# Optimization experiments

Hardware: AMD Instinct MI355X
Metric: run time of the kernel (lower is better)

## Reference

```python
import jax, jax.numpy as jnp
import numpy as np

EPS_KERNEL = 1e-6
EPS_Z = 1e-6


def softmax_kernel(data, projection_matrix):
    # data: [b,h,l,d], projection_matrix: [m,d]
    data_normalizer = data.shape[-1] ** (-0.25)
    data = data * data_normalizer
    projection = jnp.einsum('bhld,md->bhlm', data, projection_matrix)
    data_squared_norm = jnp.sum(data ** 2, axis=-1, keepdims=True) / 2
    return jnp.exp(projection - data_squared_norm + EPS_KERNEL)


def setup_inputs() -> dict:
    key = jax.random.key(0)
    k1, k2, k3, k4 = jax.random.split(key, 4)
    b, h, l, d, m = 4, 8, 8192, 64, 256
    return {
        'q': jax.random.normal(k1, (b, h, l, d), dtype=jnp.float32),
        'k': jax.random.normal(k2, (b, h, l, d), dtype=jnp.float32),
        'v': jax.random.normal(k3, (b, h, l, d), dtype=jnp.float32),
        'projection_matrix': jax.random.normal(k4, (m, d), dtype=jnp.float32),
    }


def reference(q, k, v, projection_matrix):
    q_prime = softmax_kernel(q, projection_matrix)  # [b,h,l,m]
    k_prime = softmax_kernel(k, projection_matrix)  # [b,h,l,m]
    kv = jnp.einsum('bhlm,bhld->bhmd', k_prime, v)  # [b,h,m,d]
    k_sum = jnp.sum(k_prime, axis=2)                # [b,h,m]
    z_raw = jnp.einsum('bhlm,bhm->bhl', q_prime, k_sum)
    z = 1.0 / (z_raw + EPS_Z)                       # [b,h,l]
    # (q_prime @ kv) scaled per-token by z
    out = jnp.einsum('bhlm,bhmd->bhld', q_prime, kv) * z[..., None]
    return out
```

## Files before the change

### kernel.cpp

```cpp
#include <hip/hip_runtime.h>
#include <hip/hip_bf16.h>


#define BH 32
#define LL 8192
#define DD 64
#define MM 256
#define NRM 0.35355339059327373f
#define SQS 0.0625f
#define EPSK 1e-6f
#define EPSZ 1e-6f
#define NTILE 8
#define RPB 256

typedef __attribute__((ext_vector_type(8))) short bf16x8;
typedef __attribute__((ext_vector_type(4))) float f32x4;
#define MFMA(a, b, c) __builtin_amdgcn_mfma_f32_16x16x32_bf16(a, b, c, 0, 0, 0)

static __device__ __forceinline__ short f2bf(float x) {
    union { float f; unsigned u; } c{x};
    unsigned r = c.u + 0x7fffu + ((c.u >> 16) & 1u);
    return (short)(r >> 16);
}

static __device__ __forceinline__ void decode_block(int i, int& bh, int& chunk) {
    bh = ((i & 7) << 2) | ((i >> 3) & 3);
    chunk = i >> 5;
}

static __device__ __forceinline__ void load_pfrags(
    const float* __restrict__ Pm, int wv, int quad, int l16, bf16x8 pb[2][4])
{
#pragma unroll
    for (int ks = 0; ks < 2; ++ks)
#pragma unroll
        for (int mt = 0; mt < 4; ++mt) {
            const float* pr = Pm + (wv * 64 + mt * 16 + l16) * DD + ks * 32 + quad * 8;
            float4 p0 = *(const float4*)pr;
            float4 p1 = *(const float4*)(pr + 4);
            bf16x8 f;
            f[0] = f2bf(p0.x * NRM); f[1] = f2bf(p0.y * NRM);
            f[2] = f2bf(p0.z * NRM); f[3] = f2bf(p0.w * NRM);
            f[4] = f2bf(p1.x * NRM); f[5] = f2bf(p1.y * NRM);
            f[6] = f2bf(p1.z * NRM); f[7] = f2bf(p1.w * NRM);
            pb[ks][mt] = f;
        }
}

__global__ __launch_bounds__(256, 2) void kv_kernel(
    const float* __restrict__ kin, const float* __restrict__ vin,
    const float* __restrict__ Pm, float* __restrict__ kv, float* __restrict__ ksum)
{
    __shared__ short Kb[32 * 72];
    __shared__ short Vt[64 * 40];
    __shared__ short Ktp[256 * 40];
    __shared__ float cl_lds[32];

    const int t = threadIdx.x;
    const int lane = t & 63, wv = t >> 6;
    const int quad = lane >> 4, l16 = lane & 15;
    const int bh = blockIdx.x >> 4, chunk = blockIdx.x & 15;

    bf16x8 pb[2][4];
    load_pfrags(Pm, wv, quad, l16, pb);

    f32x4 kvacc[4][4];
#pragma unroll
    for (int mt = 0; mt < 4; ++mt)
#pragma unroll
        for (int dt = 0; dt < 4; ++dt) kvacc[mt][dt] = (f32x4)0.f;
    float ksacc[4] = {0.f, 0.f, 0.f, 0.f};

    const size_t base = ((size_t)bh * LL + (size_t)chunk * 512) * DD;
    const float* kb = kin + base;
    const float* vb = vin + base;
    const int sl = t >> 4, sd4 = t & 15;

    for (int tile = 0; tile < 16; ++tile) {
        __syncthreads();
#pragma unroll
        for (int half = 0; half < 2; ++half) {
            const int l = sl + half * 16;
            const int gi = (tile * 32 + l) * DD + sd4 * 4;
            float4 kf = *(const float4*)(kb + gi);
            float sq = kf.x * kf.x + kf.y * kf.y + kf.z * kf.z + kf.w * kf.w;
            sq += __shfl_xor(sq, 1); sq += __shfl_xor(sq, 2);
            sq += __shfl_xor(sq, 4); sq += __shfl_xor(sq, 8);
            if (sd4 == 0) cl_lds[l] = EPSK - SQS * sq;
            union { short s[4]; unsigned long long u; } uk;
            uk.s[0] = f2bf(kf.x); uk.s[1] = f2bf(kf.y);
            uk.s[2] = f2bf(kf.z); uk.s[3] = f2bf(kf.w);
            *(unsigned long long*)&Kb[l * 72 + sd4 * 4] = uk.u;
            float4 vf = *(const float4*)(vb + gi);
            Vt[(sd4 * 4 + 0) * 40 + l] = f2bf(vf.x);
            Vt[(sd4 * 4 + 1) * 40 + l] = f2bf(vf.y);
            Vt[(sd4 * 4 + 2) * 40 + l] = f2bf(vf.z);
            Vt[(sd4 * 4 + 3) * 40 + l] = f2bf(vf.w);
        }
        __syncthreads();
        f32x4 pt[2][4];
#pragma unroll
        for (int lt = 0; lt < 2; ++lt)
#pragma unroll
            for (int mt = 0; mt < 4; ++mt) pt[lt][mt] = (f32x4)0.f;
#pragma unroll
        for (int ks = 0; ks < 2; ++ks)
#pragma unroll
            for (int lt = 0; lt < 2; ++lt) {
                bf16x8 af = *(bf16x8*)&Kb[(lt * 16 + l16) * 72 + ks * 32 + quad * 8];
#pragma unroll
                for (int mt = 0; mt < 4; ++mt)
                    pt[lt][mt] = MFMA(af, pb[ks][mt], pt[lt][mt]);
            }
        float cl[2][4];
#pragma unroll
        for (int lt = 0; lt < 2; ++lt)
#pragma unroll
            for (int r = 0; r < 4; ++r) cl[lt][r] = cl_lds[lt * 16 + quad * 4 + r];
#pragma unroll
        for (int lt = 0; lt < 2; ++lt)
#pragma unroll
            for (int mt = 0; mt < 4; ++mt) {
                union { short s[4]; unsigned long long u; } uo;
#pragma unroll
                for (int r = 0; r < 4; ++r) {
                    float w = __expf(pt[lt][mt][r] + cl[lt][r]);
                    ksacc[mt] += w;
                    uo.s[r] = f2bf(w);
                }
                *(unsigned long long*)&Ktp[(wv * 64 + mt * 16 + l16) * 40 + lt * 16 + quad * 4] = uo.u;
            }
        bf16x8 aK[4], bV[4];
#pragma unroll
        for (int mt = 0; mt < 4; ++mt)
            aK[mt] = *(bf16x8*)&Ktp[(wv * 64 + mt * 16 + l16) * 40 + quad * 8];
#pragma unroll
        for (int dt = 0; dt < 4; ++dt)
            bV[dt] = *(bf16x8*)&Vt[(dt * 16 + l16) * 40 + quad * 8];
#pragma unroll
        for (int mt = 0; mt < 4; ++mt)
#pragma unroll
            for (int dt = 0; dt < 4; ++dt)
                kvacc[mt][dt] = MFMA(aK[mt], bV[dt], kvacc[mt][dt]);
    }
    float* kvg = kv + (size_t)bh * MM * DD;
#pragma unroll
    for (int mt = 0; mt < 4; ++mt) {
        float r = ksacc[mt];
        r += __shfl_xor(r, 16); r += __shfl_xor(r, 32);
        if (quad == 0) atomicAdd(ksum + bh * MM + wv * 64 + mt * 16 + l16, r);
#pragma unroll
        for (int dt = 0; dt < 4; ++dt)
#pragma unroll
            for (int rg = 0; rg < 4; ++rg)
                atomicAdd(kvg + (wv * 64 + mt * 16 + quad * 4 + rg) * DD + dt * 16 + l16,
                          kvacc[mt][dt][rg]);
    }
}

__global__ __launch_bounds__(256, 4) void out_kernel(
    const float* __restrict__ qin, const float* __restrict__ Pm,
    const float* __restrict__ kv, const float* __restrict__ ksum,
    float* __restrict__ out)
{
    __shared__ short sm[64 * 264];
    __shared__ short Qb[32 * 72];
    __shared__ float ks_lds[MM];
    __shared__ float cl_lds[32];
    __shared__ float z_lds[32];

    const int t = threadIdx.x;
    const int lane = t & 63, wv = t >> 6;
    const int quad = lane >> 4, l16 = lane & 15;
    int bh, chunk;
    decode_block(blockIdx.x, bh, chunk);

    bf16x8 pb[2][4];
    load_pfrags(Pm, wv, quad, l16, pb);

    const float* kvg = kv + (size_t)bh * MM * DD;
#pragma unroll
    for (int it = 0; it < 16; ++it) {
        const int i = t + it * 256;
        const int m = i >> 4, d4 = i & 15;
        const float4 f = *(const float4*)(kvg + m * DD + d4 * 4);
        sm[(d4 * 4 + 0) * 264 + m] = f2bf(f.x);
        sm[(d4 * 4 + 1) * 264 + m] = f2bf(f.y);
        sm[(d4 * 4 + 2) * 264 + m] = f2bf(f.z);
        sm[(d4 * 4 + 3) * 264 + m] = f2bf(f.w);
    }
    ks_lds[t] = ksum[bh * MM + t];
    __syncthreads();

    bf16x8 bk[8];
#pragma unroll
    for (int ks = 0; ks < 8; ++ks)
        bk[ks] = *(const bf16x8*)&sm[(wv * 16 + l16) * 264 + ks * 32 + quad * 8];

    const size_t base = ((size_t)bh * LL + (size_t)chunk * RPB) * DD;
    const float* qb = qin + base;
    float* ob = out + base;
    const int sl = t >> 4, sd4 = t & 15;

    float4 qreg[2];
#pragma unroll
    for (int half = 0; half < 2; ++half)
        qreg[half] = *(const float4*)(qb + (sl + half * 16) * DD + sd4 * 4);

    for (int tile = 0; tile < NTILE; ++tile) {
        __syncthreads();
        if (t < 32) z_lds[t] = 0.f;
#pragma unroll
        for (int half = 0; half < 2; ++half) {
            const int l = sl + half * 16;
            const float4 qf = qreg[half];
            float sq = qf.x * qf.x + qf.y * qf.y + qf.z * qf.z + qf.w * qf.w;
            sq += __shfl_xor(sq, 1); sq += __shfl_xor(sq, 2);
            sq += __shfl_xor(sq, 4); sq += __shfl_xor(sq, 8);
            if (sd4 == 0) cl_lds[l] = EPSK - SQS * sq;
            union { short s[4]; unsigned long long u; } uq;
            uq.s[0] = f2bf(qf.x); uq.s[1] = f2bf(qf.y);
            uq.s[2] = f2bf(qf.z); uq.s[3] = f2bf(qf.w);
            *(unsigned long long*)&Qb[l * 72 + sd4 * 4] = uq.u;
        }
        if (tile + 1 < NTILE) {
#pragma unroll
            for (int half = 0; half < 2; ++half)
                qreg[half] = *(const float4*)(qb + ((tile + 1) * 32 + sl + half * 16) * DD + sd4 * 4);
        }
        __syncthreads();

        bf16x8 qf2[2][2];
#pragma unroll
        for (int ks2 = 0; ks2 < 2; ++ks2)
#pragma unroll
            for (int lt = 0; lt < 2; ++lt)
                qf2[ks2][lt] = *(const bf16x8*)&Qb[(lt * 16 + l16) * 72 + ks2 * 32 + quad * 8];
        const float clv0 = cl_lds[l16];
        const float clv1 = cl_lds[16 + l16];
        float zp0 = 0.f, zp1 = 0.f;
#pragma unroll
        for (int mt = 0; mt < 4; ++mt) {
            f32x4 pt0 = (f32x4)0.f, pt1 = (f32x4)0.f;
#pragma unroll
            for (int ks2 = 0; ks2 < 2; ++ks2) {
                pt0 = MFMA(pb[ks2][mt], qf2[ks2][0], pt0);
                pt1 = MFMA(pb[ks2][mt], qf2[ks2][1], pt1);
            }
            const float4 km4 = *(const float4*)&ks_lds[wv * 64 + mt * 16 + quad * 4];
            const float km[4] = {km4.x, km4.y, km4.z, km4.w};
            union { short s[4]; unsigned long long u; } u0, u1;
#pragma unroll
            for (int r = 0; r < 4; ++r) {
                const float w0 = __expf(pt0[r] + clv0);
                const float w1 = __expf(pt1[r] + clv1);
                zp0 += w0 * km[r];
                zp1 += w1 * km[r];
                u0.s[r] = f2bf(w0);
                u1.s[r] = f2bf(w1);
            }
            *(unsigned long long*)&sm[(l16) * 264 + wv * 64 + mt * 16 + quad * 4] = u0.u;
            *(unsigned long long*)&sm[(16 + l16) * 264 + wv * 64 + mt * 16 + quad * 4] = u1.u;
        }
        zp0 += __shfl_xor(zp0, 16); zp0 += __shfl_xor(zp0, 32);
        zp1 += __shfl_xor(zp1, 16); zp1 += __shfl_xor(zp1, 32);
        if (lane < 16) {
            atomicAdd(&z_lds[l16], zp0);
            atomicAdd(&z_lds[16 + l16], zp1);
        }
        __syncthreads();

        f32x4 oc0 = (f32x4)0.f, oc1 = (f32x4)0.f;
#pragma unroll
        for (int ks = 0; ks < 8; ++ks) {
            const bf16x8 aq0 = *(const bf16x8*)&sm[(l16) * 264 + ks * 32 + quad * 8];
            const bf16x8 aq1 = *(const bf16x8*)&sm[(16 + l16) * 264 + ks * 32 + quad * 8];
            oc0 = MFMA(aq0, bk[ks], oc0);
            oc1 = MFMA(aq1, bk[ks], oc1);
        }
#pragma unroll
        for (int r = 0; r < 4; ++r) {
            const int row0 = quad * 4 + r;
            const float z0 = 1.f / (z_lds[row0] + EPSZ);
            ob[(size_t)(tile * 32 + row0) * DD + wv * 16 + l16] = oc0[r] * z0;
            const int row1 = 16 + quad * 4 + r;
            const float z1 = 1.f / (z_lds[row1] + EPSZ);
            ob[(size_t)(tile * 32 + row1) * DD + wv * 16 + l16] = oc1[r] * z1;
        }
    }
}

extern "C" void kernel_launch(void* const* d_in, const int* in_sizes, int n_in,
                              void* d_out, int out_size, void* d_ws, size_t ws_size,
                              hipStream_t stream) {
    const float* q  = (const float*)d_in[0];
    const float* k  = (const float*)d_in[1];
    const float* v  = (const float*)d_in[2];
    const float* Pm = (const float*)d_in[3];

    float* kvw = (float*)d_ws;
    float* ksw = kvw + (size_t)BH * MM * DD;

    hipMemsetAsync(d_ws, 0, ((size_t)BH * MM * DD + (size_t)BH * MM) * sizeof(float), stream);
    hipLaunchKernelGGL(kv_kernel, dim3(512), dim3(256), 0, stream, k, v, Pm, kvw, ksw);
    hipLaunchKernelGGL(out_kernel, dim3(1024), dim3(256), 0, stream, q, Pm, kvw, ksw, (float*)d_out);
}
```

Baseline: 327.0 us.

## Replace atomic kv accumulation with per-block partials and a reduction kernel

Each kv block now writes its partial kv and k_sum results to a dedicated workspace slice instead of accumulating into a zeroed buffer. A separate reduce kernel then sums the 16 chunk partials per head. This removes the memset and the contended global accumulation. The cost is an extra kernel launch and significant extra global memory traffic for the partials. The new path only runs when the workspace is large enough, otherwise it falls back to the old path.

```diff
diff --git a/kernel.cpp b/kernel.cpp
--- a/kernel.cpp
+++ b/kernel.cpp
@@ -13,6 +13,13 @@
 #define NTILE 8
 #define RPB 256
 
+#define NBLK_A 512
+#define KVP_SZ ((size_t)NBLK_A * MM * DD)
+#define KSP_SZ ((size_t)NBLK_A * MM)
+#define KVF_SZ ((size_t)BH * MM * DD)
+#define KSF_SZ ((size_t)BH * MM)
+#define WS_NEED_BYTES ((KVP_SZ + KSP_SZ + KVF_SZ + KSF_SZ) * sizeof(float))
+
 typedef __attribute__((ext_vector_type(8))) short bf16x8;
 typedef __attribute__((ext_vector_type(4))) float f32x4;
 #define MFMA(a, b, c) __builtin_amdgcn_mfma_f32_16x16x32_bf16(a, b, c, 0, 0, 0)
@@ -45,6 +52,154 @@
             f[6] = f2bf(p1.z * NRM); f[7] = f2bf(p1.w * NRM);
             pb[ks][mt] = f;
         }
+}
+
+__global__ __launch_bounds__(256, 2) void kv_partial_kernel(
+    const float* __restrict__ kin, const float* __restrict__ vin,
+    const float* __restrict__ Pm, float* __restrict__ kvp, float* __restrict__ ksp)
+{
+    __shared__ short Kb[32 * 72];
+    __shared__ short Vt[64 * 40];
+    __shared__ short Ktp[256 * 40];
+    __shared__ float cl_lds[32];
+
+    const int t = threadIdx.x;
+    const int lane = t & 63, wv = t >> 6;
+    const int quad = lane >> 4, l16 = lane & 15;
+    const int bh = blockIdx.x >> 4, chunk = blockIdx.x & 15;
+
+    bf16x8 pb[2][4];
+    load_pfrags(Pm, wv, quad, l16, pb);
+
+    f32x4 kvacc[4][4];
+#pragma unroll
+    for (int mt = 0; mt < 4; ++mt)
+#pragma unroll
+        for (int dt = 0; dt < 4; ++dt) kvacc[mt][dt] = (f32x4)0.f;
+    float ksacc[4] = {0.f, 0.f, 0.f, 0.f};
+
+    const size_t base = ((size_t)bh * LL + (size_t)chunk * 512) * DD;
+    const float* kb = kin + base;
+    const float* vb = vin + base;
+    const int sl = t >> 4, sd4 = t & 15;
+
+    float4 kreg[2], vreg[2];
+#pragma unroll
+    for (int half = 0; half < 2; ++half) {
+        const int gi = (sl + half * 16) * DD + sd4 * 4;
+        kreg[half] = *(const float4*)(kb + gi);
+        vreg[half] = *(const float4*)(vb + gi);
+    }
+
+    for (int tile = 0; tile < 16; ++tile) {
+        __syncthreads();
+#pragma unroll
+        for (int half = 0; half < 2; ++half) {
+            const int l = sl + half * 16;
+            const float4 kf = kreg[half];
+            const float4 vf = vreg[half];
+            float sq = kf.x * kf.x + kf.y * kf.y + kf.z * kf.z + kf.w * kf.w;
+            sq += __shfl_xor(sq, 1); sq += __shfl_xor(sq, 2);
+            sq += __shfl_xor(sq, 4); sq += __shfl_xor(sq, 8);
+            if (sd4 == 0) cl_lds[l] = EPSK - SQS * sq;
+            union { short s[4]; unsigned long long u; } uk;
+            uk.s[0] = f2bf(kf.x); uk.s[1] = f2bf(kf.y);
+            uk.s[2] = f2bf(kf.z); uk.s[3] = f2bf(kf.w);
+            *(unsigned long long*)&Kb[l * 72 + sd4 * 4] = uk.u;
+            Vt[(sd4 * 4 + 0) * 40 + l] = f2bf(vf.x);
+            Vt[(sd4 * 4 + 1) * 40 + l] = f2bf(vf.y);
+            Vt[(sd4 * 4 + 2) * 40 + l] = f2bf(vf.z);
+            Vt[(sd4 * 4 + 3) * 40 + l] = f2bf(vf.w);
+        }
+        __syncthreads();
+        if (tile + 1 < 16) {
+#pragma unroll
+            for (int half = 0; half < 2; ++half) {
+                const int gi = ((tile + 1) * 32 + sl + half * 16) * DD + sd4 * 4;
+                kreg[half] = *(const float4*)(kb + gi);
+                vreg[half] = *(const float4*)(vb + gi);
+            }
+        }
+        f32x4 pt[2][4];
+#pragma unroll
+        for (int lt = 0; lt < 2; ++lt)
+#pragma unroll
+            for (int mt = 0; mt < 4; ++mt) pt[lt][mt] = (f32x4)0.f;
+#pragma unroll
+        for (int ks = 0; ks < 2; ++ks)
+#pragma unroll
+            for (int lt = 0; lt < 2; ++lt) {
+                bf16x8 af = *(bf16x8*)&Kb[(lt * 16 + l16) * 72 + ks * 32 + quad * 8];
+#pragma unroll
+                for (int mt = 0; mt < 4; ++mt)
+                    pt[lt][mt] = MFMA(af, pb[ks][mt], pt[lt][mt]);
+            }
+        float cl[2][4];
+#pragma unroll
+        for (int lt = 0; lt < 2; ++lt)
+#pragma unroll
+            for (int r = 0; r < 4; ++r) cl[lt][r] = cl_lds[lt * 16 + quad * 4 + r];
+#pragma unroll
+        for (int lt = 0; lt < 2; ++lt)
+#pragma unroll
+            for (int mt = 0; mt < 4; ++mt) {
+                union { short s[4]; unsigned long long u; } uo;
+#pragma unroll
+                for (int r = 0; r < 4; ++r) {
+                    float w = __expf(pt[lt][mt][r] + cl[lt][r]);
+                    ksacc[mt] += w;
+                    uo.s[r] = f2bf(w);
+                }
+                *(unsigned long long*)&Ktp[(wv * 64 + mt * 16 + l16) * 40 + lt * 16 + quad * 4] = uo.u;
+            }
+        bf16x8 aK[4], bV[4];
+#pragma unroll
+        for (int mt = 0; mt < 4; ++mt)
+            aK[mt] = *(bf16x8*)&Ktp[(wv * 64 + mt * 16 + l16) * 40 + quad * 8];
+#pragma unroll
+        for (int dt = 0; dt < 4; ++dt)
+            bV[dt] = *(bf16x8*)&Vt[(dt * 16 + l16) * 40 + quad * 8];
+#pragma unroll
+        for (int mt = 0; mt < 4; ++mt)
+#pragma unroll
+            for (int dt = 0; dt < 4; ++dt)
+                kvacc[mt][dt] = MFMA(aK[mt], bV[dt], kvacc[mt][dt]);
+    }
+    float* kvb = kvp + (size_t)blockIdx.x * (MM * DD);
+#pragma unroll
+    for (int mt = 0; mt < 4; ++mt) {
+        float r = ksacc[mt];
+        r += __shfl_xor(r, 16); r += __shfl_xor(r, 32);
+        if (quad == 0) ksp[blockIdx.x * MM + wv * 64 + mt * 16 + l16] = r;
+#pragma unroll
+        for (int dt = 0; dt < 4; ++dt)
+#pragma unroll
+            for (int rg = 0; rg < 4; ++rg)
+                kvb[(wv * 64 + mt * 16 + quad * 4 + rg) * DD + dt * 16 + l16] =
+                    kvacc[mt][dt][rg];
+    }
+}
+
+__global__ __launch_bounds__(256, 2) void reduce_kernel(
+    const float* __restrict__ kvp, const float* __restrict__ ksp,
+    float* __restrict__ kvf, float* __restrict__ ksf)
+{
+    const int t = threadIdx.x;
+    const int bh = blockIdx.x >> 4, s = blockIdx.x & 15;
+    const int i = s * 1024 + t * 4;
+    float4 acc = make_float4(0.f, 0.f, 0.f, 0.f);
+#pragma unroll
+    for (int c = 0; c < 16; ++c) {
+        const float4 p = *(const float4*)&kvp[((size_t)(bh * 16 + c)) * (MM * DD) + i];
+        acc.x += p.x; acc.y += p.y; acc.z += p.z; acc.w += p.w;
+    }
+    *(float4*)&kvf[(size_t)bh * (MM * DD) + i] = acc;
+    if (s == 0) {
+        float a = 0.f;
+#pragma unroll
+        for (int c = 0; c < 16; ++c) a += ksp[(bh * 16 + c) * MM + t];
+        ksf[bh * MM + t] = a;
+    }
 }
 
 __global__ __launch_bounds__(256, 2) void kv_kernel(
@@ -298,10 +453,22 @@
     const float* v  = (const float*)d_in[2];
     const float* Pm = (const float*)d_in[3];
 
-    float* kvw = (float*)d_ws;
-    float* ksw = kvw + (size_t)BH * MM * DD;
-
-    hipMemsetAsync(d_ws, 0, ((size_t)BH * MM * DD + (size_t)BH * MM) * sizeof(float), stream);
-    hipLaunchKernelGGL(kv_kernel, dim3(512), dim3(256), 0, stream, k, v, Pm, kvw, ksw);
-    hipLaunchKernelGGL(out_kernel, dim3(1024), dim3(256), 0, stream, q, Pm, kvw, ksw, (float*)d_out);
-}
+    if (ws_size >= WS_NEED_BYTES) {
+        float* kvp = (float*)d_ws;
+        float* ksp = kvp + KVP_SZ;
+        float* kvf = ksp + KSP_SZ;
+        float* ksf = kvf + KVF_SZ;
+        hipLaunchKernelGGL(kv_partial_kernel, dim3(NBLK_A), dim3(256), 0, stream,
+                           k, v, Pm, kvp, ksp);
+        hipLaunchKernelGGL(reduce_kernel, dim3(512), dim3(256), 0, stream,
+                           kvp, ksp, kvf, ksf);
+        hipLaunchKernelGGL(out_kernel, dim3(1024), dim3(256), 0, stream,
+                           q, Pm, kvf, ksf, (float*)d_out);
+    } else {
+        float* kvw = (float*)d_ws;
+        float* ksw = kvw + (size_t)BH * MM * DD;
+        hipMemsetAsync(d_ws, 0, ((size_t)BH * MM * DD + (size_t)BH * MM) * sizeof(float), stream);
+        hipLaunchKernelGGL(kv_kernel, dim3(512), dim3(256), 0, stream, k, v, Pm, kvw, ksw);
+        hipLaunchKernelGGL(out_kernel, dim3(1024), dim3(256), 0, stream, q, Pm, kvw, ksw, (float*)d_out);
+    }
+}
```

Result: faster. 293.0 us (-10.4%).
